# Performance work log

Measured on AMD Instinct MI355X. Metric: run time of the kernel, lower is better.

The kernel has to match this reference:

```python
import jax, jax.numpy as jnp
import numpy as np

N_NODES = 100000
N_EDGES = 1600000
IN_DIM = 512
HID = 64
OUT_DIM = 5


def _gcn_conv(x, row, col, w, W, b, n_nodes):
    """PyG GCNConv: h = x @ W; out[col] += norm * h[row]; out += b.
    norm = deg^-1/2[row] * w * deg^-1/2[col], deg from edge weights scattered on col,
    with self-loops (weight 1) already appended by caller."""
    h = x @ W  # [N, F_out]
    deg = jax.ops.segment_sum(w, col, num_segments=n_nodes)  # [N]
    dinv = jnp.where(deg > 0, jax.lax.rsqrt(deg), 0.0)
    norm = dinv[row] * w * dinv[col]  # [E']
    msg = h[row] * norm[:, None]  # [E', F_out] edge-wise gather + scale
    out = jax.ops.segment_sum(msg, col, num_segments=n_nodes)  # scatter-add
    return out + b


def setup_inputs() -> dict:
    key = jax.random.key(0)
    ks = jax.random.split(key, 10)
    x = jax.random.normal(ks[0], (N_NODES, IN_DIM), dtype=jnp.float32)
    edge_index = jax.random.randint(ks[1], (2, N_EDGES), 0, N_NODES, dtype=jnp.int32)
    edge_attr = jax.random.uniform(ks[2], (N_EDGES,), dtype=jnp.float32)
    # Glorot-ish init for params
    W1 = jax.random.normal(ks[3], (IN_DIM, HID), dtype=jnp.float32) * (1.0 / np.sqrt(IN_DIM))
    b1 = jnp.zeros((HID,), dtype=jnp.float32)
    W2 = jax.random.normal(ks[4], (HID, HID), dtype=jnp.float32) * (1.0 / np.sqrt(HID))
    b2 = jnp.zeros((HID,), dtype=jnp.float32)
    Wfc = jax.random.normal(ks[5], (HID, OUT_DIM), dtype=jnp.float32) * (1.0 / np.sqrt(HID))
    bfc = jnp.zeros((OUT_DIM,), dtype=jnp.float32)
    return {"x": x, "edge_index": edge_index, "edge_attr": edge_attr,
            "W1": W1, "b1": b1, "W2": W2, "b2": b2, "Wfc": Wfc, "bfc": bfc}


def reference(x, edge_index, edge_attr, W1, b1, W2, b2, Wfc, bfc):
    n = x.shape[0]
    loop = jnp.arange(n, dtype=edge_index.dtype)
    row = jnp.concatenate([edge_index[0], loop])  # source nodes + self-loops
    col = jnp.concatenate([edge_index[1], loop])  # target nodes + self-loops
    w = jnp.concatenate([edge_attr, jnp.ones((n,), dtype=edge_attr.dtype)])
    h = jax.nn.relu(_gcn_conv(x, row, col, w, W1, b1, n))
    # dropout(p=0.5) is identity in eval/reference mode
    h = jax.nn.relu(_gcn_conv(h, row, col, w, W2, b2, n))
    return h @ Wfc + bfc
```

## Files before the change

kernel.cpp:

```cpp
#include <hip/hip_runtime.h>

#define HID 64
#define OUTD 5
#define BCAP 16384
#define PART_CHUNK 4096

typedef __attribute__((ext_vector_type(8))) short bf16x8;
typedef __attribute__((ext_vector_type(4))) float f32x4;

__device__ inline void split_bf16(float x, short& hi, short& lo) {
    unsigned u = __float_as_uint(x);
    unsigned h = u >> 16;
    float hf = __uint_as_float(h << 16);
    float lof = x - hf;
    unsigned l = __float_as_uint(lof) >> 16;
    hi = (short)h; lo = (short)l;
}

__device__ inline ushort f2bf(float x) {
    unsigned u = __float_as_uint(x);
    u += 0x7fffu + ((u >> 16) & 1u);
    return (ushort)(u >> 16);
}

__global__ void k_prep(const float* __restrict__ W1, const float* __restrict__ W2,
                       short* __restrict__ w1hi, short* __restrict__ w1lo,
                       short* __restrict__ w2hi, short* __restrict__ w2lo,
                       int* __restrict__ gcursor, int nbuck) {
    int gid = blockIdx.x * blockDim.x + threadIdx.x;
    if (gid < nbuck) gcursor[gid] = 0;
    if (gid >= 32768 + 4096) return;
    int which = (gid >= 32768);
    int g = which ? gid - 32768 : gid;
    const float* W = which ? W2 : W1;
    short* ph = which ? w2hi : w1hi;
    short* pl = which ? w2lo : w1lo;
    int b = g & 7, lane = (g >> 3) & 63, c = (g >> 9) & 3, s = g >> 11;
    int k = s * 32 + 8 * (lane >> 4) + b;
    int j = c * 16 + (lane & 15);
    float x = W[k * 64 + j];
    short hi, lo; split_bf16(x, hi, lo);
    ph[g] = hi; pl[g] = lo;
}

__device__ inline void gemm1_body(const float* __restrict__ A,
                                  const short* __restrict__ whi,
                                  const short* __restrict__ wlo,
                                  ushort* __restrict__ C, int M, int bid, int tid) {
    const int K = 512, NS = 16;
    int lane = tid & 63;
    int wave = tid >> 6;
    int r0 = bid * 128 + wave * 32;

    int ar0 = r0 + (lane & 15);      if (ar0 >= M) ar0 = M - 1;
    int ar1 = r0 + 16 + (lane & 15); if (ar1 >= M) ar1 = M - 1;
    const float* pa0 = A + (size_t)ar0 * K + 8 * (lane >> 4);
    const float* pa1 = A + (size_t)ar1 * K + 8 * (lane >> 4);
    const bf16x8* bh = (const bf16x8*)whi + lane;
    const bf16x8* bl = (const bf16x8*)wlo + lane;

    f32x4 acc[2][4];
    #pragma unroll
    for (int r = 0; r < 2; r++)
        #pragma unroll
        for (int c = 0; c < 4; c++) acc[r][c] = (f32x4){0.f, 0.f, 0.f, 0.f};

    #pragma unroll
    for (int s = 0; s < NS; s++) {
        float4 x0 = *(const float4*)(pa0 + s * 32);
        float4 x1 = *(const float4*)(pa0 + s * 32 + 4);
        float4 y0 = *(const float4*)(pa1 + s * 32);
        float4 y1 = *(const float4*)(pa1 + s * 32 + 4);
        float xs[8] = {x0.x, x0.y, x0.z, x0.w, x1.x, x1.y, x1.z, x1.w};
        float ys[8] = {y0.x, y0.y, y0.z, y0.w, y1.x, y1.y, y1.z, y1.w};
        bf16x8 ah0, al0, ah1, al1;
        #pragma unroll
        for (int e = 0; e < 8; e++) {
            short h, l;
            split_bf16(xs[e], h, l); ah0[e] = h; al0[e] = l;
            split_bf16(ys[e], h, l); ah1[e] = h; al1[e] = l;
        }
        #pragma unroll
        for (int c = 0; c < 4; c++) {
            bf16x8 wh = bh[(s * 4 + c) * 64];
            bf16x8 wl = bl[(s * 4 + c) * 64];
            acc[0][c] = __builtin_amdgcn_mfma_f32_16x16x32_bf16(ah0, wh, acc[0][c], 0, 0, 0);
            acc[0][c] = __builtin_amdgcn_mfma_f32_16x16x32_bf16(ah0, wl, acc[0][c], 0, 0, 0);
            acc[0][c] = __builtin_amdgcn_mfma_f32_16x16x32_bf16(al0, wh, acc[0][c], 0, 0, 0);
            acc[1][c] = __builtin_amdgcn_mfma_f32_16x16x32_bf16(ah1, wh, acc[1][c], 0, 0, 0);
            acc[1][c] = __builtin_amdgcn_mfma_f32_16x16x32_bf16(ah1, wl, acc[1][c], 0, 0, 0);
            acc[1][c] = __builtin_amdgcn_mfma_f32_16x16x32_bf16(al1, wh, acc[1][c], 0, 0, 0);
        }
    }

    #pragma unroll
    for (int r = 0; r < 2; r++) {
        #pragma unroll
        for (int reg = 0; reg < 4; reg++) {
            int grow = r0 + r * 16 + 4 * (lane >> 4) + reg;
            if (grow < M) {
                #pragma unroll
                for (int c = 0; c < 4; c++)
                    C[(size_t)grow * 64 + c * 16 + (lane & 15)] = f2bf(acc[r][c][reg]);
            }
        }
    }
}

__global__ __launch_bounds__(256) void k_fused1(const float* __restrict__ x,
                                                const short* __restrict__ w1hi,
                                                const short* __restrict__ w1lo,
                                                ushort* __restrict__ h1, int M, int gGemm,
                                                const int* __restrict__ row,
                                                const int* __restrict__ col,
                                                const float* __restrict__ ea,
                                                int* __restrict__ gcursor,
                                                int2* __restrict__ bucket_mem,
                                                int nbuck, int E) {
    __shared__ int sh[512];
    int bid = blockIdx.x;
    int t = threadIdx.x;
    if (bid < gGemm) {
        gemm1_body(x, w1hi, w1lo, h1, M, bid, t);
        return;
    }
    int* hist = sh;
    int* basearr = sh + 256;
    int pb = bid - gGemm;
    int e0 = pb * PART_CHUNK;
    if (t < nbuck) hist[t] = 0;
    __syncthreads();
    int cols[PART_CHUNK / 256];
    #pragma unroll
    for (int i = 0; i < PART_CHUNK / 256; i++) {
        int e = e0 + t + i * 256;
        cols[i] = (e < E) ? col[e] : -1;
        if (cols[i] >= 0) atomicAdd(&hist[cols[i] >> 9], 1);
    }
    __syncthreads();
    if (t < nbuck) {
        basearr[t] = atomicAdd(&gcursor[t], hist[t]);
        hist[t] = 0;
    }
    __syncthreads();
    #pragma unroll
    for (int i = 0; i < PART_CHUNK / 256; i++) {
        int e = e0 + t + i * 256;
        if (e < E) {
            int c = cols[i];
            int b = c >> 9;
            int pos = basearr[b] + atomicAdd(&hist[b], 1);
            if (pos < BCAP) {
                int pack = ((c & 511) << 17) | row[e];
                bucket_mem[(size_t)b * BCAP + pos] = make_int2(pack, __float_as_int(ea[e]));
            }
        }
    }
}

__global__ __launch_bounds__(256) void k_build(const int* __restrict__ gcursor,
                                               const int2* __restrict__ bucket_mem,
                                               int2* __restrict__ edges,
                                               int2* __restrict__ nodemeta,
                                               float* __restrict__ dinv,
                                               int* __restrict__ used, int n) {
    __shared__ int hcnt[512];
    __shared__ int hoff[512];
    __shared__ float hdeg[512];
    __shared__ int ps[256];
    int b = blockIdx.x;
    int t = threadIdx.x;
    int cntb = gcursor[b]; if (cntb > BCAP) cntb = BCAP;
    const int2* bm = bucket_mem + (size_t)b * BCAP;

    #pragma unroll
    for (int l = t; l < 512; l += 256) { hcnt[l] = 0; hdeg[l] = 0.f; }
    __syncthreads();
    for (int i = t; i < cntb; i += 256) atomicAdd(&hcnt[bm[i].x >> 17], 1);
    __syncthreads();
    int c0 = hcnt[2 * t], c1 = hcnt[2 * t + 1];
    int q0 = (c0 + 15) & ~15; if (q0 < 16) q0 = 16;
    int q1 = (c1 + 15) & ~15; if (q1 < 16) q1 = 16;
    ps[t] = q0 + q1;
    __syncthreads();
    for (int o = 1; o < 256; o <<= 1) {
        int v = (t >= o) ? ps[t - o] : 0;
        __syncthreads();
        ps[t] += v;
        __syncthreads();
    }
    int excl = ps[t] - (q0 + q1);
    hoff[2 * t] = excl;
    hoff[2 * t + 1] = excl + q0;
    if (t == 255) used[b] = ps[255];
    __syncthreads();
    #pragma unroll
    for (int l = t; l < 512; l += 256) hcnt[l] = 0;
    __syncthreads();
    for (int i = t; i < cntb; i += 256) {
        int2 eM = bm[i];
        int local = eM.x >> 17;
        int src = eM.x & 0x1FFFF;
        int p = hoff[local] + atomicAdd(&hcnt[local], 1);
        edges[(size_t)b * BCAP + p] = make_int2(src, eM.y);
        atomicAdd(&hdeg[local], __int_as_float(eM.y));
    }
    __syncthreads();
    #pragma unroll
    for (int l = t; l < 512; l += 256) {
        int node = b * 512 + l;
        if (node < n) {
            int cnt = hcnt[l];
            int pc = (cnt + 15) & ~15; if (pc < 16) pc = 16;
            for (int p2 = cnt; p2 < pc; p2++)
                edges[(size_t)b * BCAP + hoff[l] + p2] = make_int2(node, 0);
            nodemeta[node] = make_int2(b * BCAP + hoff[l], pc);
            dinv[node] = rsqrtf(hdeg[l] + 1.0f);
        }
    }
}

__global__ void k_norm2(int2* __restrict__ edges, const float* __restrict__ dinv,
                        const int* __restrict__ used, int n, int nbuck) {
    int gid = blockIdx.x * blockDim.x + threadIdx.x;
    int b = gid >> 14;
    if (b >= nbuck) return;
    int slot = gid & (BCAP - 1);
    if (slot >= used[b]) return;
    size_t idx = (size_t)b * BCAP + slot;
    int2 c = edges[idx];
    if ((unsigned)c.x < (unsigned)n) {
        c.y = __float_as_int(dinv[c.x] * __int_as_float(c.y));
        edges[idx] = c;
    }
}

template<int FC>
__global__ void k_gather4(const ushort* __restrict__ h, const int2* __restrict__ nodemeta,
                          const int2* __restrict__ edges, const float* __restrict__ dinv,
                          const float* __restrict__ bias, const float* __restrict__ Wfc,
                          const float* __restrict__ bfc, ushort* __restrict__ outb,
                          float* __restrict__ outf, int n) {
    int gw = (blockIdx.x * blockDim.x + threadIdx.x) >> 6;
    int lane = threadIdx.x & 63;
    int s = lane & 15;
    int node = gw * 4 + (lane >> 4);
    bool valid = (node < n);
    if (!valid) node = n - 1;

    int2 meta = nodemeta[node];
    int cnt = meta.y;
    const int2* seg = edges + meta.x;
    uint2 self_u = *(const uint2*)&h[(size_t)node * 64 + 4 * s];
    float dvc = dinv[node];
    int mc = max(cnt, __shfl_xor(cnt, 16));
    mc = max(mc, __shfl_xor(mc, 32));

    float a0 = 0.f, a1 = 0.f, a2 = 0.f, a3 = 0.f;
    for (int i = 0; i < mc; i += 16) {
        int base = (i < cnt) ? i : (cnt - 16);
        float live = (i < cnt) ? 1.f : 0.f;
        int4 m[8];
        #pragma unroll
        for (int q = 0; q < 8; q++) m[q] = *(const int4*)(seg + base + 2 * q);
        uint2 v[16];
        #pragma unroll
        for (int q = 0; q < 8; q++) {
            v[2 * q]     = *(const uint2*)&h[(size_t)m[q].x * 64 + 4 * s];
            v[2 * q + 1] = *(const uint2*)&h[(size_t)m[q].z * 64 + 4 * s];
        }
        #pragma unroll
        for (int q = 0; q < 8; q++) {
            float w0 = __int_as_float(m[q].y) * live;
            float w1 = __int_as_float(m[q].w) * live;
            uint2 va = v[2 * q], vb = v[2 * q + 1];
            a0 += w0 * __uint_as_float(va.x << 16);
            a1 += w0 * __uint_as_float(va.x & 0xffff0000u);
            a2 += w0 * __uint_as_float(va.y << 16);
            a3 += w0 * __uint_as_float(va.y & 0xffff0000u);
            a0 += w1 * __uint_as_float(vb.x << 16);
            a1 += w1 * __uint_as_float(vb.x & 0xffff0000u);
            a2 += w1 * __uint_as_float(vb.y << 16);
            a3 += w1 * __uint_as_float(vb.y & 0xffff0000u);
        }
    }

    float4 bv = *(const float4*)&bias[4 * s];
    float dd = dvc * dvc;
    float r0 = fmaxf(dvc * a0 + dd * __uint_as_float(self_u.x << 16) + bv.x, 0.f);
    float r1 = fmaxf(dvc * a1 + dd * __uint_as_float(self_u.x & 0xffff0000u) + bv.y, 0.f);
    float r2 = fmaxf(dvc * a2 + dd * __uint_as_float(self_u.y << 16) + bv.z, 0.f);
    float r3 = fmaxf(dvc * a3 + dd * __uint_as_float(self_u.y & 0xffff0000u) + bv.w, 0.f);

    if (FC == 0) {
        if (valid) {
            uint lo = ((uint)f2bf(r1) << 16) | (uint)f2bf(r0);
            uint hi = ((uint)f2bf(r3) << 16) | (uint)f2bf(r2);
            *(uint2*)&outb[(size_t)node * 64 + 4 * s] = make_uint2(lo, hi);
        }
    } else {
        #pragma unroll
        for (int j = 0; j < OUTD; j++) {
            float p = r0 * Wfc[(4 * s) * OUTD + j] + r1 * Wfc[(4 * s + 1) * OUTD + j]
                    + r2 * Wfc[(4 * s + 2) * OUTD + j] + r3 * Wfc[(4 * s + 3) * OUTD + j];
            #pragma unroll
            for (int o = 1; o <= 8; o <<= 1) p += __shfl_xor(p, o);
            if (s == j && valid) outf[(size_t)node * OUTD + j] = p + bfc[j];
        }
    }
}

__global__ __launch_bounds__(256) void k_gemm2(const ushort* __restrict__ A,
                                               const short* __restrict__ whi,
                                               const short* __restrict__ wlo,
                                               ushort* __restrict__ C, int M) {
    int tid = threadIdx.x;
    int lane = tid & 63;
    int wave = tid >> 6;
    int r0 = blockIdx.x * 128 + wave * 32;

    int ar0 = r0 + (lane & 15);      if (ar0 >= M) ar0 = M - 1;
    int ar1 = r0 + 16 + (lane & 15); if (ar1 >= M) ar1 = M - 1;
    const ushort* pa0 = A + (size_t)ar0 * 64 + 8 * (lane >> 4);
    const ushort* pa1 = A + (size_t)ar1 * 64 + 8 * (lane >> 4);
    const bf16x8* bh = (const bf16x8*)whi + lane;
    const bf16x8* bl = (const bf16x8*)wlo + lane;

    f32x4 acc[2][4];
    #pragma unroll
    for (int r = 0; r < 2; r++)
        #pragma unroll
        for (int c = 0; c < 4; c++) acc[r][c] = (f32x4){0.f, 0.f, 0.f, 0.f};

    #pragma unroll
    for (int s = 0; s < 2; s++) {
        bf16x8 a0 = *(const bf16x8*)(pa0 + s * 32);
        bf16x8 a1 = *(const bf16x8*)(pa1 + s * 32);
        #pragma unroll
        for (int c = 0; c < 4; c++) {
            bf16x8 wh = bh[(s * 4 + c) * 64];
            bf16x8 wl = bl[(s * 4 + c) * 64];
            acc[0][c] = __builtin_amdgcn_mfma_f32_16x16x32_bf16(a0, wh, acc[0][c], 0, 0, 0);
            acc[0][c] = __builtin_amdgcn_mfma_f32_16x16x32_bf16(a0, wl, acc[0][c], 0, 0, 0);
            acc[1][c] = __builtin_amdgcn_mfma_f32_16x16x32_bf16(a1, wh, acc[1][c], 0, 0, 0);
            acc[1][c] = __builtin_amdgcn_mfma_f32_16x16x32_bf16(a1, wl, acc[1][c], 0, 0, 0);
        }
    }

    #pragma unroll
    for (int r = 0; r < 2; r++) {
        #pragma unroll
        for (int reg = 0; reg < 4; reg++) {
            int grow = r0 + r * 16 + 4 * (lane >> 4) + reg;
            if (grow < M) {
                #pragma unroll
                for (int c = 0; c < 4; c++)
                    C[(size_t)grow * 64 + c * 16 + (lane & 15)] = f2bf(acc[r][c][reg]);
            }
        }
    }
}

extern "C" void kernel_launch(void* const* d_in, const int* in_sizes, int n_in,
                              void* d_out, int out_size, void* d_ws, size_t ws_size,
                              hipStream_t stream) {
    const float* x   = (const float*)d_in[0];
    const int*   ei  = (const int*)d_in[1];
    const float* ea  = (const float*)d_in[2];
    const float* W1  = (const float*)d_in[3];
    const float* b1  = (const float*)d_in[4];
    const float* W2  = (const float*)d_in[5];
    const float* b2  = (const float*)d_in[6];
    const float* Wfc = (const float*)d_in[7];
    const float* bfc = (const float*)d_in[8];

    const int N = in_sizes[0] / 512;
    const int E = in_sizes[1] / 2;
    const int nbuck = (N + 511) >> 9;

    const int* row = ei;
    const int* col = ei + E;

    uintptr_t p = (uintptr_t)d_ws;
    auto carve = [&](size_t bytes) -> void* {
        void* r = (void*)p;
        p += (bytes + 255) & ~(size_t)255;
        return r;
    };
    int*    gcursor    = (int*)carve((size_t)nbuck * 4);
    int*    used       = (int*)carve((size_t)nbuck * 4);
    float*  dinv       = (float*)carve((size_t)N * 4);
    int2*   nodemeta   = (int2*)carve((size_t)N * 8);
    int2*   bucket_mem = (int2*)carve((size_t)nbuck * BCAP * 8);
    int2*   edges      = (int2*)carve((size_t)nbuck * BCAP * 8);
    short*  w1hi       = (short*)carve(32768 * 2);
    short*  w1lo       = (short*)carve(32768 * 2);
    short*  w2hi       = (short*)carve(4096 * 2);
    short*  w2lo       = (short*)carve(4096 * 2);
    ushort* hbuf       = (ushort*)carve((size_t)N * 64 * 2);
    ushort* abuf       = (ushort*)carve((size_t)N * 64 * 2);
    (void)ws_size;

    const int B = 256;
    int gGemm  = (N + 127) / 128;
    int gPart  = (E + PART_CHUNK - 1) / PART_CHUNK;
    int gNorm  = nbuck * (BCAP / B);
    int gGath  = (((N + 3) / 4) * 64 + B - 1) / B;
    int gPrep  = (32768 + 4096 + B - 1) / B;

    k_prep<<<gPrep, B, 0, stream>>>(W1, W2, w1hi, w1lo, w2hi, w2lo, gcursor, nbuck);
    k_fused1<<<gGemm + gPart, B, 0, stream>>>(x, w1hi, w1lo, hbuf, N, gGemm,
                                              row, col, ea, gcursor, bucket_mem, nbuck, E);
    k_build<<<nbuck, B, 0, stream>>>(gcursor, bucket_mem, edges, nodemeta, dinv, used, N);
    k_norm2<<<gNorm, B, 0, stream>>>(edges, dinv, used, N, nbuck);
    k_gather4<0><<<gGath, B, 0, stream>>>(hbuf, nodemeta, edges, dinv, b1,
                                          nullptr, nullptr, abuf, nullptr, N);
    k_gemm2<<<gGemm, B, 0, stream>>>(abuf, w2hi, w2lo, hbuf, N);
    k_gather4<1><<<gGath, B, 0, stream>>>(hbuf, nodemeta, edges, dinv, b2,
                                          Wfc, bfc, nullptr, (float*)d_out, N);
}
```

Baseline: 244.6 us.

## Reschedule GEMM1 alongside build/normalise and fuse layer-1 gather into GEMM2

Partitioning now runs alone, and the big layer-1 GEMM is split in two halves that share launches with the bucket build and the edge-normalisation passes, so that memory-bound graph preprocessing overlaps compute-bound GEMM work. The layer-1 gather/aggregate is fused into the layer-2 GEMM through an LDS tile, which removes the intermediate activation buffer round trip and one launch. The edge normalisation now handles 4096 slots per block instead of one slot per thread. The trade-offs are higher LDS use and serial gather rounds inside the GEMM blocks, and the split GEMM may leave load imbalance between blocks.

```diff
diff --git a/kernel.cpp b/kernel.cpp
--- a/kernel.cpp
+++ b/kernel.cpp
@@ -4,6 +4,7 @@
 #define OUTD 5
 #define BCAP 16384
 #define PART_CHUNK 4096
+#define ATS 72
 
 typedef __attribute__((ext_vector_type(8))) short bf16x8;
 typedef __attribute__((ext_vector_type(4))) float f32x4;
@@ -107,27 +108,16 @@
     }
 }
 
-__global__ __launch_bounds__(256) void k_fused1(const float* __restrict__ x,
-                                                const short* __restrict__ w1hi,
-                                                const short* __restrict__ w1lo,
-                                                ushort* __restrict__ h1, int M, int gGemm,
-                                                const int* __restrict__ row,
-                                                const int* __restrict__ col,
-                                                const float* __restrict__ ea,
-                                                int* __restrict__ gcursor,
-                                                int2* __restrict__ bucket_mem,
-                                                int nbuck, int E) {
-    __shared__ int sh[512];
-    int bid = blockIdx.x;
+__global__ __launch_bounds__(256) void k_part(const int* __restrict__ row,
+                                              const int* __restrict__ col,
+                                              const float* __restrict__ ea,
+                                              int* __restrict__ gcursor,
+                                              int2* __restrict__ bucket_mem,
+                                              int nbuck, int E) {
+    __shared__ int hist[256];
+    __shared__ int basearr[256];
     int t = threadIdx.x;
-    if (bid < gGemm) {
-        gemm1_body(x, w1hi, w1lo, h1, M, bid, t);
-        return;
-    }
-    int* hist = sh;
-    int* basearr = sh + 256;
-    int pb = bid - gGemm;
-    int e0 = pb * PART_CHUNK;
+    int e0 = blockIdx.x * PART_CHUNK;
     if (t < nbuck) hist[t] = 0;
     __syncthreads();
     int cols[PART_CHUNK / 256];
@@ -158,18 +148,12 @@
     }
 }
 
-__global__ __launch_bounds__(256) void k_build(const int* __restrict__ gcursor,
-                                               const int2* __restrict__ bucket_mem,
-                                               int2* __restrict__ edges,
-                                               int2* __restrict__ nodemeta,
-                                               float* __restrict__ dinv,
-                                               int* __restrict__ used, int n) {
-    __shared__ int hcnt[512];
-    __shared__ int hoff[512];
-    __shared__ float hdeg[512];
-    __shared__ int ps[256];
-    int b = blockIdx.x;
-    int t = threadIdx.x;
+__device__ inline void build_body(const int* __restrict__ gcursor,
+                                  const int2* __restrict__ bucket_mem,
+                                  int2* __restrict__ edges, int2* __restrict__ nodemeta,
+                                  float* __restrict__ dinv, int* __restrict__ used,
+                                  int n, int b, int t,
+                                  int* hcnt, int* hoff, float* hdeg, int* ps) {
     int cntb = gcursor[b]; if (cntb > BCAP) cntb = BCAP;
     const int2* bm = bucket_mem + (size_t)b * BCAP;
 
@@ -220,34 +204,68 @@
     }
 }
 
-__global__ void k_norm2(int2* __restrict__ edges, const float* __restrict__ dinv,
-                        const int* __restrict__ used, int n, int nbuck) {
-    int gid = blockIdx.x * blockDim.x + threadIdx.x;
-    int b = gid >> 14;
-    if (b >= nbuck) return;
-    int slot = gid & (BCAP - 1);
-    if (slot >= used[b]) return;
-    size_t idx = (size_t)b * BCAP + slot;
-    int2 c = edges[idx];
-    if ((unsigned)c.x < (unsigned)n) {
-        c.y = __float_as_int(dinv[c.x] * __int_as_float(c.y));
-        edges[idx] = c;
-    }
-}
-
-template<int FC>
-__global__ void k_gather4(const ushort* __restrict__ h, const int2* __restrict__ nodemeta,
-                          const int2* __restrict__ edges, const float* __restrict__ dinv,
-                          const float* __restrict__ bias, const float* __restrict__ Wfc,
-                          const float* __restrict__ bfc, ushort* __restrict__ outb,
-                          float* __restrict__ outf, int n) {
-    int gw = (blockIdx.x * blockDim.x + threadIdx.x) >> 6;
-    int lane = threadIdx.x & 63;
-    int s = lane & 15;
-    int node = gw * 4 + (lane >> 4);
-    bool valid = (node < n);
-    if (!valid) node = n - 1;
-
+__global__ __launch_bounds__(256) void k_fusedA(const float* __restrict__ x,
+                                                const short* __restrict__ w1hi,
+                                                const short* __restrict__ w1lo,
+                                                ushort* __restrict__ h1, int M, int gH,
+                                                const int* __restrict__ gcursor,
+                                                const int2* __restrict__ bucket_mem,
+                                                int2* __restrict__ edges,
+                                                int2* __restrict__ nodemeta,
+                                                float* __restrict__ dinv,
+                                                int* __restrict__ used, int n) {
+    __shared__ int hcnt[512];
+    __shared__ int hoff[512];
+    __shared__ float hdeg[512];
+    __shared__ int ps[256];
+    int bid = blockIdx.x;
+    if (bid < gH) {
+        gemm1_body(x, w1hi, w1lo, h1, M, bid, threadIdx.x);
+    } else {
+        build_body(gcursor, bucket_mem, edges, nodemeta, dinv, used, n,
+                   bid - gH, threadIdx.x, hcnt, hoff, hdeg, ps);
+    }
+}
+
+__global__ __launch_bounds__(256) void k_fusedB(const float* __restrict__ x,
+                                                const short* __restrict__ w1hi,
+                                                const short* __restrict__ w1lo,
+                                                ushort* __restrict__ h1, int M,
+                                                int gH, int gG2,
+                                                int2* __restrict__ edges,
+                                                const float* __restrict__ dinv,
+                                                const int* __restrict__ used, int n) {
+    int bid = blockIdx.x;
+    int t = threadIdx.x;
+    if (bid < gG2) {
+        gemm1_body(x, w1hi, w1lo, h1, M, bid + gH, t);
+    } else {
+        int nb = bid - gG2;
+        int b = nb >> 2;
+        int sl0 = (nb & 3) * 4096;
+        int u = used[b];
+        #pragma unroll
+        for (int i = 0; i < 16; i++) {
+            int slot = sl0 + t + i * 256;
+            if (slot < u) {
+                size_t idx = (size_t)b * BCAP + slot;
+                int2 c = edges[idx];
+                if ((unsigned)c.x < (unsigned)n) {
+                    c.y = __float_as_int(dinv[c.x] * __int_as_float(c.y));
+                    edges[idx] = c;
+                }
+            }
+        }
+    }
+}
+
+__device__ inline void gather_core(const ushort* __restrict__ h,
+                                   const int2* __restrict__ nodemeta,
+                                   const int2* __restrict__ edges,
+                                   const float* __restrict__ dinv,
+                                   const float* __restrict__ bias,
+                                   int node, int s, float& r0, float& r1,
+                                   float& r2, float& r3) {
     int2 meta = nodemeta[node];
     int cnt = meta.y;
     const int2* seg = edges + meta.x;
@@ -287,42 +305,42 @@
 
     float4 bv = *(const float4*)&bias[4 * s];
     float dd = dvc * dvc;
-    float r0 = fmaxf(dvc * a0 + dd * __uint_as_float(self_u.x << 16) + bv.x, 0.f);
-    float r1 = fmaxf(dvc * a1 + dd * __uint_as_float(self_u.x & 0xffff0000u) + bv.y, 0.f);
-    float r2 = fmaxf(dvc * a2 + dd * __uint_as_float(self_u.y << 16) + bv.z, 0.f);
-    float r3 = fmaxf(dvc * a3 + dd * __uint_as_float(self_u.y & 0xffff0000u) + bv.w, 0.f);
-
-    if (FC == 0) {
-        if (valid) {
-            uint lo = ((uint)f2bf(r1) << 16) | (uint)f2bf(r0);
-            uint hi = ((uint)f2bf(r3) << 16) | (uint)f2bf(r2);
-            *(uint2*)&outb[(size_t)node * 64 + 4 * s] = make_uint2(lo, hi);
-        }
-    } else {
-        #pragma unroll
-        for (int j = 0; j < OUTD; j++) {
-            float p = r0 * Wfc[(4 * s) * OUTD + j] + r1 * Wfc[(4 * s + 1) * OUTD + j]
-                    + r2 * Wfc[(4 * s + 2) * OUTD + j] + r3 * Wfc[(4 * s + 3) * OUTD + j];
-            #pragma unroll
-            for (int o = 1; o <= 8; o <<= 1) p += __shfl_xor(p, o);
-            if (s == j && valid) outf[(size_t)node * OUTD + j] = p + bfc[j];
-        }
-    }
-}
-
-__global__ __launch_bounds__(256) void k_gemm2(const ushort* __restrict__ A,
-                                               const short* __restrict__ whi,
-                                               const short* __restrict__ wlo,
-                                               ushort* __restrict__ C, int M) {
+    r0 = fmaxf(dvc * a0 + dd * __uint_as_float(self_u.x << 16) + bv.x, 0.f);
+    r1 = fmaxf(dvc * a1 + dd * __uint_as_float(self_u.x & 0xffff0000u) + bv.y, 0.f);
+    r2 = fmaxf(dvc * a2 + dd * __uint_as_float(self_u.y << 16) + bv.z, 0.f);
+    r3 = fmaxf(dvc * a3 + dd * __uint_as_float(self_u.y & 0xffff0000u) + bv.w, 0.f);
+}
+
+__global__ __launch_bounds__(256) void k_g0g2(const ushort* __restrict__ h,
+                                              const int2* __restrict__ nodemeta,
+                                              const int2* __restrict__ edges,
+                                              const float* __restrict__ dinv,
+                                              const float* __restrict__ bias,
+                                              const short* __restrict__ whi,
+                                              const short* __restrict__ wlo,
+                                              ushort* __restrict__ h2, int M) {
+    __shared__ ushort atile[128 * ATS];
     int tid = threadIdx.x;
     int lane = tid & 63;
     int wave = tid >> 6;
-    int r0 = blockIdx.x * 128 + wave * 32;
-
-    int ar0 = r0 + (lane & 15);      if (ar0 >= M) ar0 = M - 1;
-    int ar1 = r0 + 16 + (lane & 15); if (ar1 >= M) ar1 = M - 1;
-    const ushort* pa0 = A + (size_t)ar0 * 64 + 8 * (lane >> 4);
-    const ushort* pa1 = A + (size_t)ar1 * 64 + 8 * (lane >> 4);
+    int s = lane & 15;
+    int r0 = blockIdx.x * 128;
+
+    #pragma unroll 1
+    for (int rd = 0; rd < 8; rd++) {
+        int local = wave * 32 + rd * 4 + (lane >> 4);
+        int node = r0 + local;
+        if (node >= M) node = M - 1;
+        float v0, v1, v2, v3;
+        gather_core(h, nodemeta, edges, dinv, bias, node, s, v0, v1, v2, v3);
+        uint lo = ((uint)f2bf(v1) << 16) | (uint)f2bf(v0);
+        uint hi = ((uint)f2bf(v3) << 16) | (uint)f2bf(v2);
+        *(uint2*)&atile[local * ATS + 4 * s] = make_uint2(lo, hi);
+    }
+    __syncthreads();
+
+    const ushort* pa0 = atile + (wave * 32 + (lane & 15)) * ATS + 8 * (lane >> 4);
+    const ushort* pa1 = pa0 + 16 * ATS;
     const bf16x8* bh = (const bf16x8*)whi + lane;
     const bf16x8* bl = (const bf16x8*)wlo + lane;
 
@@ -333,13 +351,13 @@
         for (int c = 0; c < 4; c++) acc[r][c] = (f32x4){0.f, 0.f, 0.f, 0.f};
 
     #pragma unroll
-    for (int s = 0; s < 2; s++) {
-        bf16x8 a0 = *(const bf16x8*)(pa0 + s * 32);
-        bf16x8 a1 = *(const bf16x8*)(pa1 + s * 32);
+    for (int st = 0; st < 2; st++) {
+        bf16x8 a0 = *(const bf16x8*)(pa0 + st * 32);
+        bf16x8 a1 = *(const bf16x8*)(pa1 + st * 32);
         #pragma unroll
         for (int c = 0; c < 4; c++) {
-            bf16x8 wh = bh[(s * 4 + c) * 64];
-            bf16x8 wl = bl[(s * 4 + c) * 64];
+            bf16x8 wh = bh[(st * 4 + c) * 64];
+            bf16x8 wl = bl[(st * 4 + c) * 64];
             acc[0][c] = __builtin_amdgcn_mfma_f32_16x16x32_bf16(a0, wh, acc[0][c], 0, 0, 0);
             acc[0][c] = __builtin_amdgcn_mfma_f32_16x16x32_bf16(a0, wl, acc[0][c], 0, 0, 0);
             acc[1][c] = __builtin_amdgcn_mfma_f32_16x16x32_bf16(a1, wh, acc[1][c], 0, 0, 0);
@@ -347,17 +365,40 @@
         }
     }
 
+    int rbase = r0 + wave * 32;
     #pragma unroll
     for (int r = 0; r < 2; r++) {
         #pragma unroll
         for (int reg = 0; reg < 4; reg++) {
-            int grow = r0 + r * 16 + 4 * (lane >> 4) + reg;
+            int grow = rbase + r * 16 + 4 * (lane >> 4) + reg;
             if (grow < M) {
                 #pragma unroll
                 for (int c = 0; c < 4; c++)
-                    C[(size_t)grow * 64 + c * 16 + (lane & 15)] = f2bf(acc[r][c][reg]);
+                    h2[(size_t)grow * 64 + c * 16 + (lane & 15)] = f2bf(acc[r][c][reg]);
             }
         }
+    }
+}
+
+__global__ void k_gather_fc(const ushort* __restrict__ h, const int2* __restrict__ nodemeta,
+                            const int2* __restrict__ edges, const float* __restrict__ dinv,
+                            const float* __restrict__ bias, const float* __restrict__ Wfc,
+                            const float* __restrict__ bfc, float* __restrict__ outf, int n) {
+    int gw = (blockIdx.x * blockDim.x + threadIdx.x) >> 6;
+    int lane = threadIdx.x & 63;
+    int s = lane & 15;
+    int node = gw * 4 + (lane >> 4);
+    bool valid = (node < n);
+    if (!valid) node = n - 1;
+    float r0, r1, r2, r3;
+    gather_core(h, nodemeta, edges, dinv, bias, node, s, r0, r1, r2, r3);
+    #pragma unroll
+    for (int j = 0; j < OUTD; j++) {
+        float p = r0 * Wfc[(4 * s) * OUTD + j] + r1 * Wfc[(4 * s + 1) * OUTD + j]
+                + r2 * Wfc[(4 * s + 2) * OUTD + j] + r3 * Wfc[(4 * s + 3) * OUTD + j];
+        #pragma unroll
+        for (int o = 1; o <= 8; o <<= 1) p += __shfl_xor(p, o);
+        if (s == j && valid) outf[(size_t)node * OUTD + j] = p + bfc[j];
     }
 }
 
@@ -398,24 +439,27 @@
     short*  w2hi       = (short*)carve(4096 * 2);
     short*  w2lo       = (short*)carve(4096 * 2);
     ushort* hbuf       = (ushort*)carve((size_t)N * 64 * 2);
-    ushort* abuf       = (ushort*)carve((size_t)N * 64 * 2);
+    ushort* h2buf      = (ushort*)carve((size_t)N * 64 * 2);
     (void)ws_size;
 
     const int B = 256;
-    int gGemm  = (N + 127) / 128;
-    int gPart  = (E + PART_CHUNK - 1) / PART_CHUNK;
-    int gNorm  = nbuck * (BCAP / B);
-    int gGath  = (((N + 3) / 4) * 64 + B - 1) / B;
-    int gPrep  = (32768 + 4096 + B - 1) / B;
+    int gGemm = (N + 127) / 128;
+    int gH    = gGemm / 2;
+    int gG2   = gGemm - gH;
+    int gPart = (E + PART_CHUNK - 1) / PART_CHUNK;
+    int gNorm = nbuck * 4;
+    int gGath = (((N + 3) / 4) * 64 + B - 1) / B;
+    int gPrep = (32768 + 4096 + B - 1) / B;
 
     k_prep<<<gPrep, B, 0, stream>>>(W1, W2, w1hi, w1lo, w2hi, w2lo, gcursor, nbuck);
-    k_fused1<<<gGemm + gPart, B, 0, stream>>>(x, w1hi, w1lo, hbuf, N, gGemm,
-                                              row, col, ea, gcursor, bucket_mem, nbuck, E);
-    k_build<<<nbuck, B, 0, stream>>>(gcursor, bucket_mem, edges, nodemeta, dinv, used, N);
-    k_norm2<<<gNorm, B, 0, stream>>>(edges, dinv, used, N, nbuck);
-    k_gather4<0><<<gGath, B, 0, stream>>>(hbuf, nodemeta, edges, dinv, b1,
-                                          nullptr, nullptr, abuf, nullptr, N);
-    k_gemm2<<<gGemm, B, 0, stream>>>(abuf, w2hi, w2lo, hbuf, N);
-    k_gather4<1><<<gGath, B, 0, stream>>>(hbuf, nodemeta, edges, dinv, b2,
-                                          Wfc, bfc, nullptr, (float*)d_out, N);
-}
+    k_part<<<gPart, B, 0, stream>>>(row, col, ea, gcursor, bucket_mem, nbuck, E);
+    k_fusedA<<<gH + nbuck, B, 0, stream>>>(x, w1hi, w1lo, hbuf, N, gH,
+                                           gcursor, bucket_mem, edges, nodemeta,
+                                           dinv, used, N);
+    k_fusedB<<<gG2 + gNorm, B, 0, stream>>>(x, w1hi, w1lo, hbuf, N, gH, gG2,
+                                            edges, dinv, used, N);
+    k_g0g2<<<gGemm, B, 0, stream>>>(hbuf, nodemeta, edges, dinv, b1,
+                                    w2hi, w2lo, h2buf, N);
+    k_gather_fc<<<gGath, B, 0, stream>>>(h2buf, nodemeta, edges, dinv, b2,
+                                         Wfc, bfc, (float*)d_out, N);
+}
```

Measured after the change: 281.1 us. 14.9% more time.

## Split layer-1 GEMM across partition and build kernels to overlap work

Applied to the files above, without the earlier changes.

The first-layer GEMM blocks are divided in half. One half runs alongside the edge-partition blocks and the other half alongside the bucket-build blocks, which now form a single fused kernel instead of a standalone k_build launch. Partition blocks are also placed before GEMM blocks in the grid so they get scheduled first. The aim is to hide the latency-bound build stage behind compute-heavy GEMM work and fill the GPU more evenly, at the cost of larger shared-memory footprints in mixed kernels, which may reduce occupancy for the GEMM blocks.

```diff
diff --git a/kernel.cpp b/kernel.cpp
--- a/kernel.cpp
+++ b/kernel.cpp
@@ -107,26 +107,10 @@
     }
 }
 
-__global__ __launch_bounds__(256) void k_fused1(const float* __restrict__ x,
-                                                const short* __restrict__ w1hi,
-                                                const short* __restrict__ w1lo,
-                                                ushort* __restrict__ h1, int M, int gGemm,
-                                                const int* __restrict__ row,
-                                                const int* __restrict__ col,
-                                                const float* __restrict__ ea,
-                                                int* __restrict__ gcursor,
-                                                int2* __restrict__ bucket_mem,
-                                                int nbuck, int E) {
-    __shared__ int sh[512];
-    int bid = blockIdx.x;
-    int t = threadIdx.x;
-    if (bid < gGemm) {
-        gemm1_body(x, w1hi, w1lo, h1, M, bid, t);
-        return;
-    }
-    int* hist = sh;
-    int* basearr = sh + 256;
-    int pb = bid - gGemm;
+__device__ inline void part_body(const int* __restrict__ row, const int* __restrict__ col,
+                                 const float* __restrict__ ea, int* __restrict__ gcursor,
+                                 int2* __restrict__ bucket_mem, int nbuck, int E,
+                                 int pb, int t, int* hist, int* basearr) {
     int e0 = pb * PART_CHUNK;
     if (t < nbuck) hist[t] = 0;
     __syncthreads();
@@ -158,18 +142,12 @@
     }
 }
 
-__global__ __launch_bounds__(256) void k_build(const int* __restrict__ gcursor,
-                                               const int2* __restrict__ bucket_mem,
-                                               int2* __restrict__ edges,
-                                               int2* __restrict__ nodemeta,
-                                               float* __restrict__ dinv,
-                                               int* __restrict__ used, int n) {
-    __shared__ int hcnt[512];
-    __shared__ int hoff[512];
-    __shared__ float hdeg[512];
-    __shared__ int ps[256];
-    int b = blockIdx.x;
-    int t = threadIdx.x;
+__device__ inline void build_body(const int* __restrict__ gcursor,
+                                  const int2* __restrict__ bucket_mem,
+                                  int2* __restrict__ edges, int2* __restrict__ nodemeta,
+                                  float* __restrict__ dinv, int* __restrict__ used,
+                                  int n, int b, int t,
+                                  int* hcnt, int* hoff, float* hdeg, int* ps) {
     int cntb = gcursor[b]; if (cntb > BCAP) cntb = BCAP;
     const int2* bm = bucket_mem + (size_t)b * BCAP;
 
@@ -217,6 +195,50 @@
             nodemeta[node] = make_int2(b * BCAP + hoff[l], pc);
             dinv[node] = rsqrtf(hdeg[l] + 1.0f);
         }
+    }
+}
+
+__global__ __launch_bounds__(256) void k_fused1a(const float* __restrict__ x,
+                                                 const short* __restrict__ w1hi,
+                                                 const short* __restrict__ w1lo,
+                                                 ushort* __restrict__ h1, int M, int gPart,
+                                                 const int* __restrict__ row,
+                                                 const int* __restrict__ col,
+                                                 const float* __restrict__ ea,
+                                                 int* __restrict__ gcursor,
+                                                 int2* __restrict__ bucket_mem,
+                                                 int nbuck, int E) {
+    __shared__ int sh[512];
+    int bid = blockIdx.x;
+    if (bid < gPart) {
+        part_body(row, col, ea, gcursor, bucket_mem, nbuck, E, bid, threadIdx.x,
+                  sh, sh + 256);
+    } else {
+        gemm1_body(x, w1hi, w1lo, h1, M, bid - gPart, threadIdx.x);
+    }
+}
+
+__global__ __launch_bounds__(256) void k_fused1b(const float* __restrict__ x,
+                                                 const short* __restrict__ w1hi,
+                                                 const short* __restrict__ w1lo,
+                                                 ushort* __restrict__ h1, int M,
+                                                 int nbuck, int gH,
+                                                 const int* __restrict__ gcursor,
+                                                 const int2* __restrict__ bucket_mem,
+                                                 int2* __restrict__ edges,
+                                                 int2* __restrict__ nodemeta,
+                                                 float* __restrict__ dinv,
+                                                 int* __restrict__ used, int n) {
+    __shared__ int hcnt[512];
+    __shared__ int hoff[512];
+    __shared__ float hdeg[512];
+    __shared__ int ps[256];
+    int bid = blockIdx.x;
+    if (bid < nbuck) {
+        build_body(gcursor, bucket_mem, edges, nodemeta, dinv, used, n,
+                   bid, threadIdx.x, hcnt, hoff, hdeg, ps);
+    } else {
+        gemm1_body(x, w1hi, w1lo, h1, M, bid - nbuck + gH, threadIdx.x);
     }
 }
 
@@ -402,16 +424,20 @@
     (void)ws_size;
 
     const int B = 256;
-    int gGemm  = (N + 127) / 128;
-    int gPart  = (E + PART_CHUNK - 1) / PART_CHUNK;
-    int gNorm  = nbuck * (BCAP / B);
-    int gGath  = (((N + 3) / 4) * 64 + B - 1) / B;
-    int gPrep  = (32768 + 4096 + B - 1) / B;
+    int gGemm = (N + 127) / 128;
+    int gH    = gGemm / 2;
+    int gG2   = gGemm - gH;
+    int gPart = (E + PART_CHUNK - 1) / PART_CHUNK;
+    int gNorm = nbuck * (BCAP / B);
+    int gGath = (((N + 3) / 4) * 64 + B - 1) / B;
+    int gPrep = (32768 + 4096 + B - 1) / B;
 
     k_prep<<<gPrep, B, 0, stream>>>(W1, W2, w1hi, w1lo, w2hi, w2lo, gcursor, nbuck);
-    k_fused1<<<gGemm + gPart, B, 0, stream>>>(x, w1hi, w1lo, hbuf, N, gGemm,
-                                              row, col, ea, gcursor, bucket_mem, nbuck, E);
-    k_build<<<nbuck, B, 0, stream>>>(gcursor, bucket_mem, edges, nodemeta, dinv, used, N);
+    k_fused1a<<<gPart + gH, B, 0, stream>>>(x, w1hi, w1lo, hbuf, N, gPart,
+                                            row, col, ea, gcursor, bucket_mem, nbuck, E);
+    k_fused1b<<<nbuck + gG2, B, 0, stream>>>(x, w1hi, w1lo, hbuf, N, nbuck, gH,
+                                             gcursor, bucket_mem, edges, nodemeta,
+                                             dinv, used, N);
     k_norm2<<<gNorm, B, 0, stream>>>(edges, dinv, used, N, nbuck);
     k_gather4<0><<<gGath, B, 0, stream>>>(hbuf, nodemeta, edges, dinv, b1,
                                           nullptr, nullptr, abuf, nullptr, N);
```

Measured after the change: 283.4 us. 1.16x slower.

## Sort nodes into degree bins so gather wavefronts process similar-degree nodes

Applied to the files above, without the earlier changes.

Builds a per-node histogram of padded edge counts in k_build, takes a prefix sum over 64 bins in an extra k_norm2 block, and adds a k_scatter kernel that writes a permutation grouping nodes by padded degree. Both gather kernels then read their node through this permutation, so the four nodes sharing a wavefront have similar edge counts and less of the loop is spent waiting on the longest one. The cost is an extra kernel launch, global atomics on 64 bin counters, and an indirection that breaks the sequential node order of the self-feature, dinv and output accesses.

```diff
diff --git a/kernel.cpp b/kernel.cpp
--- a/kernel.cpp
+++ b/kernel.cpp
@@ -26,9 +26,11 @@
 __global__ void k_prep(const float* __restrict__ W1, const float* __restrict__ W2,
                        short* __restrict__ w1hi, short* __restrict__ w1lo,
                        short* __restrict__ w2hi, short* __restrict__ w2lo,
-                       int* __restrict__ gcursor, int nbuck) {
+                       int* __restrict__ gcursor, int nbuck,
+                       int* __restrict__ binCnt, int* __restrict__ binCur) {
     int gid = blockIdx.x * blockDim.x + threadIdx.x;
     if (gid < nbuck) gcursor[gid] = 0;
+    if (gid < 64) { binCnt[gid] = 0; binCur[gid] = 0; }
     if (gid >= 32768 + 4096) return;
     int which = (gid >= 32768);
     int g = which ? gid - 32768 : gid;
@@ -126,8 +128,7 @@
     }
     int* hist = sh;
     int* basearr = sh + 256;
-    int pb = bid - gGemm;
-    int e0 = pb * PART_CHUNK;
+    int e0 = (bid - gGemm) * PART_CHUNK;
     if (t < nbuck) hist[t] = 0;
     __syncthreads();
     int cols[PART_CHUNK / 256];
@@ -163,11 +164,13 @@
                                                int2* __restrict__ edges,
                                                int2* __restrict__ nodemeta,
                                                float* __restrict__ dinv,
-                                               int* __restrict__ used, int n) {
+                                               int* __restrict__ used,
+                                               int* __restrict__ binCnt, int n) {
     __shared__ int hcnt[512];
     __shared__ int hoff[512];
     __shared__ float hdeg[512];
     __shared__ int ps[256];
+    __shared__ int hbin[64];
     int b = blockIdx.x;
     int t = threadIdx.x;
     int cntb = gcursor[b]; if (cntb > BCAP) cntb = BCAP;
@@ -175,6 +178,7 @@
 
     #pragma unroll
     for (int l = t; l < 512; l += 256) { hcnt[l] = 0; hdeg[l] = 0.f; }
+    if (t < 64) hbin[t] = 0;
     __syncthreads();
     for (int i = t; i < cntb; i += 256) atomicAdd(&hcnt[bm[i].x >> 17], 1);
     __syncthreads();
@@ -216,12 +220,24 @@
                 edges[(size_t)b * BCAP + hoff[l] + p2] = make_int2(node, 0);
             nodemeta[node] = make_int2(b * BCAP + hoff[l], pc);
             dinv[node] = rsqrtf(hdeg[l] + 1.0f);
-        }
-    }
+            int bin = pc >> 4; if (bin > 63) bin = 63;
+            atomicAdd(&hbin[bin], 1);
+        }
+    }
+    __syncthreads();
+    if (t < 64 && hbin[t] > 0) atomicAdd(&binCnt[t], hbin[t]);
 }
 
 __global__ void k_norm2(int2* __restrict__ edges, const float* __restrict__ dinv,
-                        const int* __restrict__ used, int n, int nbuck) {
+                        const int* __restrict__ used, int n, int nbuck, int gNorm,
+                        const int* __restrict__ binCnt, int* __restrict__ binBase) {
+    if (blockIdx.x == (unsigned)gNorm) {
+        if (threadIdx.x == 0) {
+            int acc = 0;
+            for (int i = 0; i < 64; i++) { binBase[i] = acc; acc += binCnt[i]; }
+        }
+        return;
+    }
     int gid = blockIdx.x * blockDim.x + threadIdx.x;
     int b = gid >> 14;
     if (b >= nbuck) return;
@@ -235,18 +251,41 @@
     }
 }
 
+__global__ void k_scatter(const int2* __restrict__ nodemeta, const int* __restrict__ binBase,
+                          int* __restrict__ binCur, int* __restrict__ perm, int n) {
+    __shared__ int lh[64];
+    __shared__ int gb[64];
+    int t = threadIdx.x;
+    if (t < 64) lh[t] = 0;
+    __syncthreads();
+    int i = blockIdx.x * 256 + t;
+    int bin = 0, r = 0;
+    bool v = (i < n);
+    if (v) {
+        int pc = nodemeta[i].y;
+        bin = pc >> 4; if (bin > 63) bin = 63;
+        r = atomicAdd(&lh[bin], 1);
+    }
+    __syncthreads();
+    if (t < 64) gb[t] = (lh[t] > 0) ? atomicAdd(&binCur[t], lh[t]) : 0;
+    __syncthreads();
+    if (v) perm[binBase[bin] + gb[bin] + r] = i;
+}
+
 template<int FC>
 __global__ void k_gather4(const ushort* __restrict__ h, const int2* __restrict__ nodemeta,
                           const int2* __restrict__ edges, const float* __restrict__ dinv,
+                          const int* __restrict__ perm,
                           const float* __restrict__ bias, const float* __restrict__ Wfc,
                           const float* __restrict__ bfc, ushort* __restrict__ outb,
                           float* __restrict__ outf, int n) {
     int gw = (blockIdx.x * blockDim.x + threadIdx.x) >> 6;
     int lane = threadIdx.x & 63;
     int s = lane & 15;
-    int node = gw * 4 + (lane >> 4);
-    bool valid = (node < n);
-    if (!valid) node = n - 1;
+    int idx = gw * 4 + (lane >> 4);
+    bool valid = (idx < n);
+    if (!valid) idx = n - 1;
+    int node = perm[idx];
 
     int2 meta = nodemeta[node];
     int cnt = meta.y;
@@ -389,6 +428,10 @@
     };
     int*    gcursor    = (int*)carve((size_t)nbuck * 4);
     int*    used       = (int*)carve((size_t)nbuck * 4);
+    int*    binCnt     = (int*)carve(64 * 4);
+    int*    binCur     = (int*)carve(64 * 4);
+    int*    binBase    = (int*)carve(64 * 4);
+    int*    perm       = (int*)carve((size_t)N * 4);
     float*  dinv       = (float*)carve((size_t)N * 4);
     int2*   nodemeta   = (int2*)carve((size_t)N * 8);
     int2*   bucket_mem = (int2*)carve((size_t)nbuck * BCAP * 8);
@@ -402,20 +445,25 @@
     (void)ws_size;
 
     const int B = 256;
-    int gGemm  = (N + 127) / 128;
-    int gPart  = (E + PART_CHUNK - 1) / PART_CHUNK;
-    int gNorm  = nbuck * (BCAP / B);
-    int gGath  = (((N + 3) / 4) * 64 + B - 1) / B;
-    int gPrep  = (32768 + 4096 + B - 1) / B;
-
-    k_prep<<<gPrep, B, 0, stream>>>(W1, W2, w1hi, w1lo, w2hi, w2lo, gcursor, nbuck);
+    int gGemm = (N + 127) / 128;
+    int gPart = (E + PART_CHUNK - 1) / PART_CHUNK;
+    int gNorm = nbuck * (BCAP / B);
+    int gGath = (((N + 3) / 4) * 64 + B - 1) / B;
+    int gScat = (N + B - 1) / B;
+    int gPrep = (32768 + 4096 + B - 1) / B;
+
+    k_prep<<<gPrep, B, 0, stream>>>(W1, W2, w1hi, w1lo, w2hi, w2lo,
+                                    gcursor, nbuck, binCnt, binCur);
     k_fused1<<<gGemm + gPart, B, 0, stream>>>(x, w1hi, w1lo, hbuf, N, gGemm,
                                               row, col, ea, gcursor, bucket_mem, nbuck, E);
-    k_build<<<nbuck, B, 0, stream>>>(gcursor, bucket_mem, edges, nodemeta, dinv, used, N);
-    k_norm2<<<gNorm, B, 0, stream>>>(edges, dinv, used, N, nbuck);
-    k_gather4<0><<<gGath, B, 0, stream>>>(hbuf, nodemeta, edges, dinv, b1,
+    k_build<<<nbuck, B, 0, stream>>>(gcursor, bucket_mem, edges, nodemeta,
+                                     dinv, used, binCnt, N);
+    k_norm2<<<gNorm + 1, B, 0, stream>>>(edges, dinv, used, N, nbuck, gNorm,
+                                         binCnt, binBase);
+    k_scatter<<<gScat, B, 0, stream>>>(nodemeta, binBase, binCur, perm, N);
+    k_gather4<0><<<gGath, B, 0, stream>>>(hbuf, nodemeta, edges, dinv, perm, b1,
                                           nullptr, nullptr, abuf, nullptr, N);
     k_gemm2<<<gGemm, B, 0, stream>>>(abuf, w2hi, w2lo, hbuf, N);
-    k_gather4<1><<<gGath, B, 0, stream>>>(hbuf, nodemeta, edges, dinv, b2,
+    k_gather4<1><<<gGath, B, 0, stream>>>(hbuf, nodemeta, edges, dinv, perm, b2,
                                           Wfc, bfc, nullptr, (float*)d_out, N);
 }
```

After: 236.9 us. 3.1% less time.
